# Performance work log

Measured on AMD Instinct MI355X. Metric: run time of the kernel, lower is better.

## Reference

```python
import jax, jax.numpy as jnp
import numpy as np

LN_EPS = 1e-5

def setup_inputs() -> dict:
    key = jax.random.key(0)
    k0, k1, k2, k3 = jax.random.split(key, 4)
    B, N, D = 4, 4096, 512
    x = jax.random.normal(k0, (B, N, D), dtype=jnp.float32)
    s = 1.0 / np.sqrt(D)
    Wq = jax.random.normal(k1, (D, D), dtype=jnp.float32) * s
    Wk = jax.random.normal(k2, (D, D), dtype=jnp.float32) * s
    Wv = jax.random.normal(k3, (D, D), dtype=jnp.float32) * s
    gamma = jnp.ones((D,), dtype=jnp.float32)
    beta = jnp.zeros((D,), dtype=jnp.float32)
    return {"x": x, "Wq": Wq, "Wk": Wk, "Wv": Wv, "gamma": gamma, "beta": beta}

def reference(x, Wq, Wk, Wv, gamma, beta):
    # x: [B, N, D]
    D = x.shape[-1]
    q = jnp.einsum('bnd,de->bne', x, Wq)
    k = jnp.einsum('bnd,de->bne', x, Wk)
    v = jnp.einsum('bnd,de->bne', x, Wv)
    # full [B, N, N] score matrix, as in the original bmm chain
    dist = jnp.einsum('bne,bme->bnm', q, k) * (1.0 / jnp.sqrt(jnp.float32(D)))
    dist = jax.nn.softmax(dist, axis=-1)
    att = jnp.einsum('bnm,bmd->bnd', dist, v)
    # residual + LayerNorm over last dim
    h = att + x
    mu = jnp.mean(h, axis=-1, keepdims=True)
    var = jnp.mean(jnp.square(h - mu), axis=-1, keepdims=True)
    out = (h - mu) * jax.lax.rsqrt(var + LN_EPS) * gamma + beta
    return out
```

## Files before the change

kernel.cpp:

```cpp
#include <hip/hip_runtime.h>
#include <stdint.h>

typedef __attribute__((ext_vector_type(8))) __bf16 bf16x8;
typedef __attribute__((ext_vector_type(4))) float f32x4;
typedef unsigned short u16;
typedef unsigned char u8;
typedef unsigned int u32;
typedef unsigned long long u64;
typedef long i64;

#define LN_EPS 1e-5f

__device__ __forceinline__ float bf2f(u16 u){
  union { u32 i; float f; } v; v.i = ((u32)u) << 16; return v.f;
}
__device__ __forceinline__ u16 f2bf(float f){
  union { float f; u32 i; } v; v.f = f;
  u32 u = v.i;
  u += 0x7fffu + ((u >> 16) & 1u);
  return (u16)(u >> 16);
}
__device__ __forceinline__ u32 cvt_pk_fp8(float a, float b){
  u32 pk;
  asm("v_cvt_pk_fp8_f32 %0, %1, %2" : "=v"(pk) : "v"(a), "v"(b));
  return pk;
}

__device__ __forceinline__ void gload_lds16(const void* g, void* l) {
  __builtin_amdgcn_global_load_lds(
      (const __attribute__((address_space(1))) void*)g,
      (__attribute__((address_space(3))) void*)l, 16, 0, 0);
}

__global__ void xcast_kernel(const float* __restrict__ X, u16* __restrict__ Xb) {
  int idx = (blockIdx.x * 256 + threadIdx.x) * 8;
  float4 f0 = *(const float4*)&X[idx];
  float4 f1 = *(const float4*)&X[idx + 4];
  ushort4 lo, hi;
  lo.x = f2bf(f0.x); lo.y = f2bf(f0.y); lo.z = f2bf(f0.z); lo.w = f2bf(f0.w);
  hi.x = f2bf(f1.x); hi.y = f2bf(f1.y); hi.z = f2bf(f1.z); hi.w = f2bf(f1.w);
  *(ushort4*)&Xb[idx] = lo;
  *(ushort4*)&Xb[idx + 4] = hi;
}

__global__ void transpose_w_kernel(const float* __restrict__ Wq,
                                   const float* __restrict__ Wk,
                                   const float* __restrict__ Wv,
                                   u16* __restrict__ Wt) {
  const float* W = (blockIdx.y == 0) ? Wq : ((blockIdx.y == 1) ? Wk : Wv);
  u16* o = Wt + blockIdx.y * 512 * 512;
  int idx = blockIdx.x * 256 + threadIdx.x;
  int e = idx >> 9, d = idx & 511;
  o[e * 512 + d] = f2bf(W[d * 512 + e]);
}

__launch_bounds__(256, 4)
__global__ void qkv_gemm_kernel(const u16* __restrict__ Xb,
                                const u16* __restrict__ Wt,
                                u8* __restrict__ Qo,
                                u8* __restrict__ Ko,
                                u8* __restrict__ Vto8) {
  const int z = blockIdx.y;
  const u16* Wtm = Wt + z * 512 * 512;
  const int mblk = blockIdx.x & 127;
  const int nblk = blockIdx.x >> 7;
  const int m0 = mblk * 128, n0 = nblk * 128;

  __shared__ __align__(16) u8 As[128 * 64];
  __shared__ __align__(16) u8 Bs[128 * 64];

  const int tid = threadIdx.x;
  const int lane = tid & 63, w = tid >> 6;
  const int wr = w >> 1, wc = w & 1;
  const int lrow = lane & 15, quad = lane >> 4;

  f32x4 acc[4][4];
#pragma unroll
  for (int i = 0; i < 4; i++)
#pragma unroll
    for (int j = 0; j < 4; j++) acc[i][j] = (f32x4){0.f, 0.f, 0.f, 0.f};

  const int srow = lane >> 2;
  const int spos = lane & 3;

#pragma unroll
  for (int r2 = 0; r2 < 2; r2++) {
    int rowb = w * 32 + r2 * 16;
    int row = rowb + srow;
    int g = spos ^ (row & 3);
    gload_lds16(&Xb[(m0 + row) * 512 + g * 8], &As[rowb * 64]);
    gload_lds16(&Wtm[(n0 + row) * 512 + g * 8], &Bs[rowb * 64]);
  }

  for (int k = 0; k < 16; k++) {
    __syncthreads();
    bf16x8 a[4], b[4];
#pragma unroll
    for (int t = 0; t < 4; t++) {
      int ra = wr * 64 + t * 16 + lrow;
      a[t] = *(const bf16x8*)&As[ra * 64 + (quad ^ (ra & 3)) * 16];
      int rb = wc * 64 + t * 16 + lrow;
      b[t] = *(const bf16x8*)&Bs[rb * 64 + (quad ^ (rb & 3)) * 16];
    }
    __syncthreads();
    if (k < 15) {
      int k0n = (k + 1) * 32;
#pragma unroll
      for (int r2 = 0; r2 < 2; r2++) {
        int rowb = w * 32 + r2 * 16;
        int row = rowb + srow;
        int g = spos ^ (row & 3);
        gload_lds16(&Xb[(m0 + row) * 512 + k0n + g * 8], &As[rowb * 64]);
        gload_lds16(&Wtm[(n0 + row) * 512 + k0n + g * 8], &Bs[rowb * 64]);
      }
    }
#pragma unroll
    for (int i = 0; i < 4; i++)
#pragma unroll
      for (int j = 0; j < 4; j++)
        acc[i][j] = __builtin_amdgcn_mfma_f32_16x16x32_bf16(a[i], b[j], acc[i][j], 0, 0, 0);
  }

  if (z < 2) {
    u8* O = (z == 0) ? Qo : Ko;
#pragma unroll
    for (int i = 0; i < 4; i++) {
      int rbase = m0 + wr * 64 + i * 16 + quad * 4;
#pragma unroll
      for (int j = 0; j < 4; j++) {
        int col = n0 + wc * 64 + j * 16 + lrow;
        u32 pk01 = cvt_pk_fp8(acc[i][j][0], acc[i][j][1]);
        u32 pk23 = cvt_pk_fp8(acc[i][j][2], acc[i][j][3]);
        O[(rbase + 0) * 512 + col] = (u8)pk01;
        O[(rbase + 1) * 512 + col] = (u8)(pk01 >> 8);
        O[(rbase + 2) * 512 + col] = (u8)pk23;
        O[(rbase + 3) * 512 + col] = (u8)(pk23 >> 8);
      }
    }
  } else {
#pragma unroll
    for (int i = 0; i < 4; i++) {
      int rbase = m0 + wr * 64 + i * 16 + quad * 4;
#pragma unroll
      for (int j = 0; j < 4; j++) {
        int col = n0 + wc * 64 + j * 16 + lrow;
        u32 pk01 = cvt_pk_fp8(acc[i][j][0], acc[i][j][1]);
        u32 pk23 = cvt_pk_fp8(acc[i][j][2], acc[i][j][3]);
        u32 pk = (pk01 & 0xffffu) | (pk23 << 16);
        *(u32*)&Vto8[col * 16384 + rbase] = pk;
      }
    }
  }
}

template <int NSPLIT>
__launch_bounds__(256, 2)
__global__ void attn_partial_kernel(const u8* __restrict__ Q,
                                    const u8* __restrict__ K,
                                    const u8* __restrict__ Vt8,
                                    u16* __restrict__ Opart,
                                    float* __restrict__ L) {
  constexpr int SPAN = 4096 / NSPLIT;
  constexpr int ITERS = SPAN / 32;
  const int b = blockIdx.y;
  const int split = blockIdx.z;
  const int q0 = blockIdx.x * 64;
  const int tid = threadIdx.x;
  const int lane = tid & 63, w = tid >> 6;
  const int lrow = lane & 15, quad = lane >> 4;

  __shared__ __align__(16) u8 Ks8[2][32 * 512];
  __shared__ __align__(16) u8 Vs8[2][512 * 32];

  const int keybase = b * 4096 + split * SPAN;

  const int qtok = b * 4096 + q0 + w * 16 + lrow;
  i64 qf[16];
#pragma unroll
  for (int s = 0; s < 16; s++)
    qf[s] = *(const i64*)&Q[qtok * 512 + s * 32 + quad * 8];

  f32x4 Oacc[32];
#pragma unroll
  for (int j = 0; j < 32; j++) Oacc[j] = (f32x4){0.f, 0.f, 0.f, 0.f};

  float lsum = 0.f;
  const float scale = 0.044194173824159216f;

  auto stageK = [&](int kk, u8* Kbuf) {
#pragma unroll
    for (int i = 0; i < 4; i++) {
      int row = w * 8 + i * 2 + (lane >> 5);
      int g = (lane & 31) ^ (row & 7);
      gload_lds16(&K[(keybase + kk + row) * 512 + g * 16],
                  &Kbuf[(w * 8 + i * 2) * 512]);
    }
  };
  auto stageV = [&](int kk, u8* Vbuf) {
#pragma unroll
    for (int run = 0; run < 4; run++) {
      int rowb = w * 128 + run * 32;
      int n = rowb + (lane >> 1);
      int g16 = (lane & 1) ^ ((n >> 2) & 1);
      gload_lds16(&Vt8[n * 16384 + keybase + kk + g16 * 16], &Vbuf[rowb * 32]);
    }
  };

  stageK(0, Ks8[0]);
  stageV(0, Vs8[0]);

  for (int it = 0; it < ITERS; ++it) {
    const int cur = it & 1;
    const u8* Ksc = Ks8[cur];
    const u8* Vsc = Vs8[cur];

    __syncthreads();
    if (it < ITERS - 1) {
      stageK((it + 1) * 32, Ks8[cur ^ 1]);
      stageV((it + 1) * 32, Vs8[cur ^ 1]);
    }

    f32x4 S0 = {0.f, 0.f, 0.f, 0.f}, S1 = {0.f, 0.f, 0.f, 0.f};
#pragma unroll
    for (int s = 0; s < 16; s++) {
      int gs = (2 * s + (quad >> 1)) ^ (lrow & 7);
      int off = gs * 16 + (quad & 1) * 8;
      i64 k0 = *(const i64*)&Ksc[lrow * 512 + off];
      i64 k1 = *(const i64*)&Ksc[(16 + lrow) * 512 + off];
      S0 = __builtin_amdgcn_mfma_f32_16x16x32_fp8_fp8(k0, qf[s], S0, 0, 0, 0);
      S1 = __builtin_amdgcn_mfma_f32_16x16x32_fp8_fp8(k1, qf[s], S1, 0, 0, 0);
    }

    float p00 = __expf(S0[0] * scale), p01 = __expf(S0[1] * scale);
    float p02 = __expf(S0[2] * scale), p03 = __expf(S0[3] * scale);
    float p10 = __expf(S1[0] * scale), p11 = __expf(S1[1] * scale);
    float p12 = __expf(S1[2] * scale), p13 = __expf(S1[3] * scale);
    lsum += ((p00 + p01) + (p02 + p03)) + ((p10 + p11) + (p12 + p13));
    u32 dwA = (cvt_pk_fp8(p00, p01) & 0xffffu) | (cvt_pk_fp8(p02, p03) << 16);
    u32 dwB = (cvt_pk_fp8(p10, p11) & 0xffffu) | (cvt_pk_fp8(p12, p13) << 16);

    {
      int srcl = lrow + 32 * (quad & 1);
      u32 loA = (u32)__shfl((int)dwA, srcl);
      u32 hiA = (u32)__shfl((int)dwA, srcl + 16);
      u32 loB = (u32)__shfl((int)dwB, srcl);
      u32 hiB = (u32)__shfl((int)dwB, srcl + 16);
      u32 lo = (quad >= 2) ? loB : loA;
      u32 hi = (quad >= 2) ? hiB : hiA;
      i64 af = (i64)(((u64)hi << 32) | (u64)lo);

#pragma unroll
      for (int j = 0; j < 32; j++) {
        int n = j * 16 + lrow;
        int off = (((quad >> 1) ^ ((n >> 2) & 1)) << 4) + (quad & 1) * 8;
        i64 bv = *(const i64*)&Vsc[n * 32 + off];
        Oacc[j] = __builtin_amdgcn_mfma_f32_16x16x32_fp8_fp8(af, bv, Oacc[j], 0, 0, 0);
      }
    }
  }

  {
    float s = lsum;
    s += __shfl_xor(s, 16);
    s += __shfl_xor(s, 32);
    if (quad == 0)
      L[split * 16384 + b * 4096 + q0 + w * 16 + lrow] = s;
  }

  u16* Ob = Opart + (size_t)split * (16384u * 512u);
  const int tokr = b * 4096 + q0 + w * 16 + quad * 4;
#pragma unroll
  for (int j = 0; j < 32; j++) {
#pragma unroll
    for (int p = 0; p < 4; p++)
      Ob[(size_t)(tokr + p) * 512 + j * 16 + lrow] = f2bf(Oacc[j][p]);
  }
}

template <int NSPLIT>
__launch_bounds__(256)
__global__ void combine_ln_kernel(const u16* __restrict__ Opart,
                                  const float* __restrict__ L,
                                  const float* __restrict__ X,
                                  const float* __restrict__ gamma,
                                  const float* __restrict__ beta,
                                  float* __restrict__ Out) {
  const int lane = threadIdx.x & 63;
  const int tok = blockIdx.x * 4 + (threadIdx.x >> 6);
  float lt = 0.f;
#pragma unroll
  for (int s = 0; s < NSPLIT; s++) lt += L[s * 16384 + tok];
  const float inv_l = 1.f / lt;
  const int base = tok * 512 + lane * 8;

  float h[8] = {0.f, 0.f, 0.f, 0.f, 0.f, 0.f, 0.f, 0.f};
#pragma unroll
  for (int s = 0; s < NSPLIT; s++) {
    uint4 avec = *(const uint4*)&Opart[(size_t)s * (16384u * 512u) + base];
    const u16* ap = (const u16*)&avec;
#pragma unroll
    for (int i = 0; i < 8; i++) h[i] += bf2f(ap[i]);
  }

  float4 x0 = *(const float4*)&X[base];
  float4 x1 = *(const float4*)&X[base + 4];
  float xs[8] = {x0.x, x0.y, x0.z, x0.w, x1.x, x1.y, x1.z, x1.w};
#pragma unroll
  for (int i = 0; i < 8; i++) h[i] = h[i] * inv_l + xs[i];

  float sum = 0.f, sq = 0.f;
#pragma unroll
  for (int i = 0; i < 8; i++) { sum += h[i]; sq += h[i] * h[i]; }
#pragma unroll
  for (int d = 1; d < 64; d <<= 1) {
    sum += __shfl_xor(sum, d);
    sq  += __shfl_xor(sq, d);
  }
  float mu = sum * (1.f / 512.f);
  float var = sq * (1.f / 512.f) - mu * mu;
  float rstd = rsqrtf(var + LN_EPS);

  float4 g0 = *(const float4*)&gamma[lane * 8];
  float4 g1 = *(const float4*)&gamma[lane * 8 + 4];
  float4 b0 = *(const float4*)&beta[lane * 8];
  float4 b1 = *(const float4*)&beta[lane * 8 + 4];
  float gs[8] = {g0.x, g0.y, g0.z, g0.w, g1.x, g1.y, g1.z, g1.w};
  float bs[8] = {b0.x, b0.y, b0.z, b0.w, b1.x, b1.y, b1.z, b1.w};

  float4 o0, o1;
  float* op = (float*)&o0;
#pragma unroll
  for (int i = 0; i < 4; i++) op[i] = (h[i] - mu) * rstd * gs[i] + bs[i];
  float* op1 = (float*)&o1;
#pragma unroll
  for (int i = 0; i < 4; i++) op1[i] = (h[i + 4] - mu) * rstd * gs[i + 4] + bs[i + 4];
  *(float4*)&Out[base] = o0;
  *(float4*)&Out[base + 4] = o1;
}

extern "C" void kernel_launch(void* const* d_in, const int* in_sizes, int n_in,
                              void* d_out, int out_size, void* d_ws, size_t ws_size,
                              hipStream_t stream) {
  const float* x = (const float*)d_in[0];
  const float* Wq = (const float*)d_in[1];
  const float* Wk = (const float*)d_in[2];
  const float* Wv = (const float*)d_in[3];
  const float* gamma = (const float*)d_in[4];
  const float* beta = (const float*)d_in[5];

  char* ws = (char*)d_ws;
  u8*  Qws   = (u8*)(ws);
  u8*  Kws   = (u8*)(ws + 8388608);
  u8*  Vt8ws = (u8*)(ws + 16777216);
  u16* Wtws  = (u16*)(ws + 25165824);
  u16* Xbws  = (u16*)(ws + 26738688);
  u16* Opws  = (u16*)(ws + 26738688);
  const size_t PART = 16777216;
  float* Lws = (float*)(ws + 26738688 + 2 * PART);

  hipLaunchKernelGGL(xcast_kernel, dim3(4096), dim3(256), 0, stream, x, Xbws);
  hipLaunchKernelGGL(transpose_w_kernel, dim3(1024, 3), dim3(256), 0, stream,
                     Wq, Wk, Wv, Wtws);
  hipLaunchKernelGGL(qkv_gemm_kernel, dim3(512, 3), dim3(256), 0, stream,
                     Xbws, Wtws, Qws, Kws, Vt8ws);
  hipLaunchKernelGGL(HIP_KERNEL_NAME(attn_partial_kernel<2>),
                     dim3(64, 4, 2), dim3(256), 0, stream,
                     Qws, Kws, Vt8ws, Opws, Lws);
  hipLaunchKernelGGL(HIP_KERNEL_NAME(combine_ln_kernel<2>),
                     dim3(4096), dim3(256), 0, stream,
                     Opws, Lws, x, gamma, beta, (float*)d_out);
}
```

Baseline: 295.7 us.

## Split attention warps 2x2 over query pairs and key/value halves via LDS P exchange

```diff
diff --git a/kernel.cpp b/kernel.cpp
--- a/kernel.cpp
+++ b/kernel.cpp
@@ -168,23 +168,29 @@
   const int tid = threadIdx.x;
   const int lane = tid & 63, w = tid >> 6;
   const int lrow = lane & 15, quad = lane >> 4;
+  const int qp = w >> 1, x = w & 1;
 
   __shared__ __align__(16) u8 Ks8[2][32 * 512];
   __shared__ __align__(16) u8 Vs8[2][512 * 32];
+  __shared__ __align__(16) u8 Pb[64 * 40];
 
   const int keybase = b * 4096 + split * SPAN;
 
-  const int qtok = b * 4096 + q0 + w * 16 + lrow;
-  i64 qf[16];
-#pragma unroll
-  for (int s = 0; s < 16; s++)
-    qf[s] = *(const i64*)&Q[qtok * 512 + s * 32 + quad * 8];
-
-  f32x4 Oacc[32];
-#pragma unroll
-  for (int j = 0; j < 32; j++) Oacc[j] = (f32x4){0.f, 0.f, 0.f, 0.f};
-
-  float lsum = 0.f;
+  const int qtokb = b * 4096 + q0 + qp * 32;
+  i64 qf[2][16];
+#pragma unroll
+  for (int qg = 0; qg < 2; qg++)
+#pragma unroll
+    for (int s = 0; s < 16; s++)
+      qf[qg][s] = *(const i64*)&Q[(qtokb + qg * 16 + lrow) * 512 + s * 32 + quad * 8];
+
+  f32x4 Oacc[2][16];
+#pragma unroll
+  for (int qg = 0; qg < 2; qg++)
+#pragma unroll
+    for (int j = 0; j < 16; j++) Oacc[qg][j] = (f32x4){0.f, 0.f, 0.f, 0.f};
+
+  float lsum[2] = {0.f, 0.f};
   const float scale = 0.044194173824159216f;
 
   auto stageK = [&](int kk, u8* Kbuf) {
@@ -209,6 +215,8 @@
   stageK(0, Ks8[0]);
   stageV(0, Vs8[0]);
 
+  const int krow = x * 16 + lrow;
+
   for (int it = 0; it < ITERS; ++it) {
     const int cur = it & 1;
     const u8* Ksc = Ks8[cur];
@@ -223,58 +231,62 @@
     f32x4 S0 = {0.f, 0.f, 0.f, 0.f}, S1 = {0.f, 0.f, 0.f, 0.f};
 #pragma unroll
     for (int s = 0; s < 16; s++) {
-      int gs = (2 * s + (quad >> 1)) ^ (lrow & 7);
+      int gs = (2 * s + (quad >> 1)) ^ (krow & 7);
       int off = gs * 16 + (quad & 1) * 8;
-      i64 k0 = *(const i64*)&Ksc[lrow * 512 + off];
-      i64 k1 = *(const i64*)&Ksc[(16 + lrow) * 512 + off];
-      S0 = __builtin_amdgcn_mfma_f32_16x16x32_fp8_fp8(k0, qf[s], S0, 0, 0, 0);
-      S1 = __builtin_amdgcn_mfma_f32_16x16x32_fp8_fp8(k1, qf[s], S1, 0, 0, 0);
-    }
-
-    float p00 = __expf(S0[0] * scale), p01 = __expf(S0[1] * scale);
-    float p02 = __expf(S0[2] * scale), p03 = __expf(S0[3] * scale);
-    float p10 = __expf(S1[0] * scale), p11 = __expf(S1[1] * scale);
-    float p12 = __expf(S1[2] * scale), p13 = __expf(S1[3] * scale);
-    lsum += ((p00 + p01) + (p02 + p03)) + ((p10 + p11) + (p12 + p13));
-    u32 dwA = (cvt_pk_fp8(p00, p01) & 0xffffu) | (cvt_pk_fp8(p02, p03) << 16);
-    u32 dwB = (cvt_pk_fp8(p10, p11) & 0xffffu) | (cvt_pk_fp8(p12, p13) << 16);
+      i64 kf = *(const i64*)&Ksc[krow * 512 + off];
+      S0 = __builtin_amdgcn_mfma_f32_16x16x32_fp8_fp8(kf, qf[0][s], S0, 0, 0, 0);
+      S1 = __builtin_amdgcn_mfma_f32_16x16x32_fp8_fp8(kf, qf[1][s], S1, 0, 0, 0);
+    }
 
     {
-      int srcl = lrow + 32 * (quad & 1);
-      u32 loA = (u32)__shfl((int)dwA, srcl);
-      u32 hiA = (u32)__shfl((int)dwA, srcl + 16);
-      u32 loB = (u32)__shfl((int)dwB, srcl);
-      u32 hiB = (u32)__shfl((int)dwB, srcl + 16);
-      u32 lo = (quad >= 2) ? loB : loA;
-      u32 hi = (quad >= 2) ? hiB : hiA;
-      i64 af = (i64)(((u64)hi << 32) | (u64)lo);
-
-#pragma unroll
-      for (int j = 0; j < 32; j++) {
-        int n = j * 16 + lrow;
-        int off = (((quad >> 1) ^ ((n >> 2) & 1)) << 4) + (quad & 1) * 8;
-        i64 bv = *(const i64*)&Vsc[n * 32 + off];
-        Oacc[j] = __builtin_amdgcn_mfma_f32_16x16x32_fp8_fp8(af, bv, Oacc[j], 0, 0, 0);
-      }
-    }
-  }
-
-  {
-    float s = lsum;
+      float p0 = __expf(S0[0] * scale), p1 = __expf(S0[1] * scale);
+      float p2 = __expf(S0[2] * scale), p3 = __expf(S0[3] * scale);
+      lsum[0] += (p0 + p1) + (p2 + p3);
+      u32 dw = (cvt_pk_fp8(p0, p1) & 0xffffu) | (cvt_pk_fp8(p2, p3) << 16);
+      *(u32*)&Pb[(qp * 32 + lrow) * 40 + x * 16 + quad * 4] = dw;
+    }
+    {
+      float p0 = __expf(S1[0] * scale), p1 = __expf(S1[1] * scale);
+      float p2 = __expf(S1[2] * scale), p3 = __expf(S1[3] * scale);
+      lsum[1] += (p0 + p1) + (p2 + p3);
+      u32 dw = (cvt_pk_fp8(p0, p1) & 0xffffu) | (cvt_pk_fp8(p2, p3) << 16);
+      *(u32*)&Pb[(qp * 32 + 16 + lrow) * 40 + x * 16 + quad * 4] = dw;
+    }
+
+    __syncthreads();
+
+    i64 pa0 = *(const i64*)&Pb[(qp * 32 + lrow) * 40 + quad * 8];
+    i64 pa1 = *(const i64*)&Pb[(qp * 32 + 16 + lrow) * 40 + quad * 8];
+#pragma unroll
+    for (int j = 0; j < 16; j++) {
+      int n = x * 256 + j * 16 + lrow;
+      int off = (((quad >> 1) ^ ((n >> 2) & 1)) << 4) + (quad & 1) * 8;
+      i64 bv = *(const i64*)&Vsc[n * 32 + off];
+      Oacc[0][j] = __builtin_amdgcn_mfma_f32_16x16x32_fp8_fp8(pa0, bv, Oacc[0][j], 0, 0, 0);
+      Oacc[1][j] = __builtin_amdgcn_mfma_f32_16x16x32_fp8_fp8(pa1, bv, Oacc[1][j], 0, 0, 0);
+    }
+  }
+
+#pragma unroll
+  for (int qg = 0; qg < 2; qg++) {
+    float s = lsum[qg];
     s += __shfl_xor(s, 16);
     s += __shfl_xor(s, 32);
     if (quad == 0)
-      L[split * 16384 + b * 4096 + q0 + w * 16 + lrow] = s;
+      L[(split * 2 + x) * 16384 + b * 4096 + q0 + qp * 32 + qg * 16 + lrow] = s;
   }
 
   u16* Ob = Opart + (size_t)split * (16384u * 512u);
-  const int tokr = b * 4096 + q0 + w * 16 + quad * 4;
-#pragma unroll
-  for (int j = 0; j < 32; j++) {
-#pragma unroll
-    for (int p = 0; p < 4; p++)
-      Ob[(size_t)(tokr + p) * 512 + j * 16 + lrow] = f2bf(Oacc[j][p]);
-  }
+  const int tokb2 = b * 4096 + q0 + qp * 32;
+#pragma unroll
+  for (int qg = 0; qg < 2; qg++)
+#pragma unroll
+    for (int j = 0; j < 16; j++) {
+      int col = x * 256 + j * 16 + lrow;
+#pragma unroll
+      for (int r = 0; r < 4; r++)
+        Ob[(size_t)(tokb2 + qg * 16 + quad * 4 + r) * 512 + col] = f2bf(Oacc[qg][j][r]);
+    }
 }
 
 template <int NSPLIT>
@@ -289,7 +301,7 @@
   const int tok = blockIdx.x * 4 + (threadIdx.x >> 6);
   float lt = 0.f;
 #pragma unroll
-  for (int s = 0; s < NSPLIT; s++) lt += L[s * 16384 + tok];
+  for (int s = 0; s < 2 * NSPLIT; s++) lt += L[s * 16384 + tok];
   const float inv_l = 1.f / lt;
   const int base = tok * 512 + lane * 8;
 
```

New measurement: 287.2 us. 2.9% less time.
